# Optimization experiments

Measured on AMD Instinct MI355X. Metric: run time of the kernel, lower is better.

Reference implementation:

```python
import jax, jax.numpy as jnp
import numpy as np

N = 100000   # nodes
E = 1600000  # edges
G = 512      # graphs in batch
IN_C, H1, H2, OUT_C = 3, 64, 128, 2


def setup_inputs() -> dict:
    key = jax.random.key(0)
    ks = jax.random.split(key, 9)
    x = jax.random.normal(ks[0], (N, IN_C), dtype=jnp.float32)
    edge_index = jax.random.randint(ks[1], (2, E), 0, N, dtype=jnp.int64)
    batch = jnp.sort(jax.random.randint(ks[2], (N,), 0, G, dtype=jnp.int64))
    # Glorot-ish init for weights, zeros for biases (as PyG GCNConv / nn.Linear defaults roughly)
    def glorot(k, shape):
        lim = float(np.sqrt(6.0 / (shape[0] + shape[1])))
        return jax.random.uniform(k, shape, jnp.float32, -lim, lim)
    W1 = glorot(ks[3], (IN_C, H1)); b1 = jnp.zeros((H1,), jnp.float32)
    W2 = glorot(ks[4], (H1, H2));   b2 = jnp.zeros((H2,), jnp.float32)
    Wfc = glorot(ks[5], (H2, OUT_C)); bfc = jnp.zeros((OUT_C,), jnp.float32)
    return {"x": x, "edge_index": edge_index, "batch": batch,
            "W1": W1, "b1": b1, "W2": W2, "b2": b2, "Wfc": Wfc, "bfc": bfc}


def _gcn_conv(x, W, b, src, dst, dinv):
    # PyG GCNConv: out = D^{-1/2} (A + I) D^{-1/2} X W + b
    xw = x @ W                                    # [N, F]
    norm = dinv[src] * dinv[dst]                  # per-edge symmetric norm
    agg = jax.ops.segment_sum(norm[:, None] * xw[src], dst, num_segments=x.shape[0])
    agg = agg + (dinv * dinv)[:, None] * xw       # self-loop contribution
    return agg + b


def reference(x, edge_index, batch, W1, b1, W2, b2, Wfc, bfc):
    src, dst = edge_index[0], edge_index[1]
    # degree with self-loops (edge weight 1), counted at edge targets as in PyG
    deg = jax.ops.segment_sum(jnp.ones((E,), x.dtype), dst, num_segments=N) + 1.0
    dinv = jax.lax.rsqrt(deg)
    h = jax.nn.relu(_gcn_conv(x, W1, b1, src, dst, dinv))
    h = jax.nn.relu(_gcn_conv(h, W2, b2, src, dst, dinv))
    # global_mean_pool over batch indices
    sums = jax.ops.segment_sum(h, batch, num_segments=G)          # [G, H2]
    cnt = jax.ops.segment_sum(jnp.ones((N,), h.dtype), batch, num_segments=G)
    pooled = sums / jnp.maximum(cnt, 1.0)[:, None]
    return pooled @ Wfc + bfc
```

## Files before the change

### kernel.cpp

```cpp
#include <hip/hip_runtime.h>

#define NN 100000
#define NE 1600000
#define NG 512
#define C_H1 64
#define C_H2 128
#define C_OUT 2

#define MM2_BLOCKS ((NN + 127) / 128)
#define NB ((NN + 255) >> 8)
#define PCHUNKS 512
#define PCHUNK_E (NE / PCHUNKS)
#define AT_S 68

__global__ void k_hist(const int* __restrict__ ei, int* __restrict__ hist) {
    __shared__ int lh[NB];
    int tid = threadIdx.x;
    int blk = blockIdx.x;
    for (int i = tid; i < NB; i += 256) lh[i] = 0;
    __syncthreads();
    int base = blk * PCHUNK_E;
    for (int e = base + tid; e < base + PCHUNK_E; e += 256)
        atomicAdd(&lh[ei[NE + e] >> 8], 1);
    __syncthreads();
    for (int i = tid; i < NB; i += 256) hist[i * PCHUNKS + blk] = lh[i];
}

__global__ void k_colscan0(const int* __restrict__ hist, int* __restrict__ offs,
                           int* __restrict__ btot) {
    __shared__ int sh[256];
    int b = blockIdx.x;
    int tid = threadIdx.x;
    int v0 = hist[b * PCHUNKS + 2 * tid];
    int v1 = hist[b * PCHUNKS + 2 * tid + 1];
    sh[tid] = v0 + v1;
    __syncthreads();
    for (int off = 1; off < 256; off <<= 1) {
        int v = (tid >= off) ? sh[tid - off] : 0;
        __syncthreads();
        sh[tid] += v;
        __syncthreads();
    }
    int base = (tid == 0) ? 0 : sh[tid - 1];
    offs[b * PCHUNKS + 2 * tid]     = base;
    offs[b * PCHUNKS + 2 * tid + 1] = base + v0;
    if (tid == 255) btot[b] = sh[255];
}

__global__ void k_bbase(const int* __restrict__ btot, int* __restrict__ bbase,
                        int* __restrict__ row_ptr) {
    __shared__ int sh[256];
    int tid = threadIdx.x;
    int v0 = (2 * tid     < NB) ? btot[2 * tid]     : 0;
    int v1 = (2 * tid + 1 < NB) ? btot[2 * tid + 1] : 0;
    sh[tid] = v0 + v1;
    __syncthreads();
    for (int off = 1; off < 256; off <<= 1) {
        int v = (tid >= off) ? sh[tid - off] : 0;
        __syncthreads();
        sh[tid] += v;
        __syncthreads();
    }
    int base = (tid == 0) ? 0 : sh[tid - 1];
    if (2 * tid     < NB) bbase[2 * tid]     = base;
    if (2 * tid + 1 < NB) bbase[2 * tid + 1] = base + v0;
    if (tid == 255) { bbase[NB] = sh[255]; row_ptr[NN] = sh[255]; }
}

__global__ void k_scatterA(const int* __restrict__ ei, const int* __restrict__ offs,
                           const int* __restrict__ bbase, int2* __restrict__ ed2) {
    __shared__ int lcur[NB];
    int tid = threadIdx.x;
    int blk = blockIdx.x;
    for (int i = tid; i < NB; i += 256) lcur[i] = bbase[i] + offs[i * PCHUNKS + blk];
    __syncthreads();
    int base = blk * PCHUNK_E;
    for (int e = base + tid; e < base + PCHUNK_E; e += 256) {
        int s = ei[e], d = ei[NE + e];
        int pos = atomicAdd(&lcur[d >> 8], 1);
        int2 v; v.x = s; v.y = d;
        ed2[pos] = v;
    }
}

__global__ void k_B1(const int2* __restrict__ ed2, const int* __restrict__ bbase,
                     float* __restrict__ dinv, int* __restrict__ row_ptr) {
    __shared__ int ldeg[256];
    __shared__ int sh[256];
    int b = blockIdx.x;
    int tid = threadIdx.x;
    int lo = b << 8;
    ldeg[tid] = 0;
    __syncthreads();
    int beg = bbase[b], end = bbase[b + 1];
    for (int j = beg + tid; j < end; j += 256)
        atomicAdd(&ldeg[ed2[j].y - lo], 1);
    __syncthreads();
    int d = ldeg[tid];
    int node = lo + tid;
    if (node < NN) dinv[node] = rsqrtf((float)d + 1.0f);
    sh[tid] = d;
    __syncthreads();
    for (int off = 1; off < 256; off <<= 1) {
        int v = (tid >= off) ? sh[tid - off] : 0;
        __syncthreads();
        sh[tid] += v;
        __syncthreads();
    }
    int excl = beg + ((tid == 0) ? 0 : sh[tid - 1]);
    if (node < NN) row_ptr[node] = excl;
}

__global__ void k_x4(const float* __restrict__ x, float4* __restrict__ x4) {
    int n = blockIdx.x * blockDim.x + threadIdx.x;
    if (n >= NN) return;
    float4 v; v.x = x[n * 3]; v.y = x[n * 3 + 1]; v.z = x[n * 3 + 2]; v.w = 0.f;
    x4[n] = v;
}

__global__ void k_scatterB(const int* __restrict__ row_ptr, const int2* __restrict__ ed2,
                           const float* __restrict__ dinv, const float4* __restrict__ x4,
                           int2* __restrict__ ed, float4* __restrict__ aggx4) {
    __shared__ int   lcur[256];
    __shared__ float ldin[256];
    __shared__ float lax[256 * 3];
    int b = blockIdx.x;
    int lo = b << 8;
    int tid = threadIdx.x;
    int node = lo + tid;
    if (node <= NN) lcur[tid] = row_ptr[node < NN ? node : NN];
    else            lcur[tid] = 0;
    ldin[tid] = (node < NN) ? dinv[node] : 0.f;
    lax[tid] = 0.f; lax[256 + tid] = 0.f; lax[512 + tid] = 0.f;
    __syncthreads();
    int seg_beg = row_ptr[lo];
    int hi = lo + 256; if (hi > NN) hi = NN;
    int seg_end = row_ptr[hi];
    for (int j = seg_beg + tid; j < seg_end; j += 256) {
        int2 sd = ed2[j];
        int local = sd.y - lo;
        int pos = atomicAdd(&lcur[local], 1);
        float nrm = dinv[sd.x] * ldin[local];
        int2 v; v.x = sd.x; v.y = __float_as_int(nrm);
        ed[pos] = v;
        float4 xs = x4[sd.x];
        atomicAdd(&lax[local],       nrm * xs.x);
        atomicAdd(&lax[256 + local], nrm * xs.y);
        atomicAdd(&lax[512 + local], nrm * xs.z);
    }
    __syncthreads();
    if (node < NN) {
        float di = ldin[tid];
        float s2 = di * di;
        float4 xs = x4[node];
        float4 a;
        a.x = lax[tid]       + s2 * xs.x;
        a.y = lax[256 + tid] + s2 * xs.y;
        a.z = lax[512 + tid] + s2 * xs.z;
        a.w = 0.f;
        aggx4[node] = a;
    }
}

__global__ void k_edge1(const int* __restrict__ row_ptr, const int2* __restrict__ ed,
                        const float4* __restrict__ aggx4, const float* __restrict__ dinv,
                        const float* __restrict__ W1, const float* __restrict__ b1,
                        float* __restrict__ agg1) {
    __shared__ float4 lp[256];
    int t = blockIdx.x * 256 + threadIdx.x;
    int n = t >> 6, c = t & 63;
    int lane = threadIdx.x & 63;
    int wbase = threadIdx.x & 192;

    float w0 = W1[c], w1 = W1[64 + c], w2 = W1[128 + c], bb = b1[c];
    float4 an = aggx4[n];
    float di = dinv[n];
    float hself = fmaxf(fmaf(an.x, w0, fmaf(an.y, w1, fmaf(an.z, w2, bb))), 0.f);
    float acc = di * di * hself;

    int beg = row_ptr[n], end = row_ptr[n + 1];
    for (int base = beg; base < end; base += 64) {
        int m = end - base; if (m > 64) m = 64;
        if (lane < m) {
            int2 v = ed[base + lane];
            float4 ax = aggx4[v.x];
            float4 p; p.x = ax.x; p.y = ax.y; p.z = ax.z; p.w = __int_as_float(v.y);
            lp[wbase + lane] = p;
        }
        int e = 0;
        for (; e + 3 < m; e += 4) {
            float4 p0 = lp[wbase + e];
            float4 p1 = lp[wbase + e + 1];
            float4 p2 = lp[wbase + e + 2];
            float4 p3 = lp[wbase + e + 3];
            float h0  = fmaxf(fmaf(p0.x, w0, fmaf(p0.y, w1, fmaf(p0.z, w2, bb))), 0.f);
            float h1v = fmaxf(fmaf(p1.x, w0, fmaf(p1.y, w1, fmaf(p1.z, w2, bb))), 0.f);
            float h2v = fmaxf(fmaf(p2.x, w0, fmaf(p2.y, w1, fmaf(p2.z, w2, bb))), 0.f);
            float h3v = fmaxf(fmaf(p3.x, w0, fmaf(p3.y, w1, fmaf(p3.z, w2, bb))), 0.f);
            acc = fmaf(p0.w, h0, acc);
            acc = fmaf(p1.w, h1v, acc);
            acc = fmaf(p2.w, h2v, acc);
            acc = fmaf(p3.w, h3v, acc);
        }
        for (; e < m; ++e) {
            float4 p = lp[wbase + e];
            float h = fmaxf(fmaf(p.x, w0, fmaf(p.y, w1, fmaf(p.z, w2, bb))), 0.f);
            acc = fmaf(p.w, h, acc);
        }
    }
    agg1[t] = acc;
}

__global__ void k_mm2pool(const float* __restrict__ agg1, const float* __restrict__ W2,
                          const float* __restrict__ b2, const int* __restrict__ batch,
                          float* __restrict__ pooled) {
    __shared__ float wt[C_H1 * C_H2];
    __shared__ float at[128 * AT_S];
    __shared__ float lpool[4 * C_H2];
    int tid = threadIdx.x;
    {
        const float4* w4 = (const float4*)W2;
        float4* wl = (float4*)wt;
        for (int i = tid; i < (C_H1 * C_H2) / 4; i += 256) wl[i] = w4[i];
        const float4* a4 = (const float4*)(agg1 + (size_t)blockIdx.x * 128 * C_H1);
        for (int i = tid; i < 128 * 16; i += 256) {
            int row = i >> 4, k4 = i & 15;
            *(float4*)&at[row * AT_S + k4 * 4] = a4[i];
        }
        for (int i = tid; i < 4 * C_H2; i += 256) lpool[i] = 0.f;
    }
    __syncthreads();

    int tx = tid & 15;
    int my = tid >> 4;
    int c0 = tx * 8;
    int m0 = my * 8;

    float acc[8][8];
#pragma unroll
    for (int i = 0; i < 8; ++i)
#pragma unroll
        for (int j = 0; j < 8; ++j) acc[i][j] = 0.f;

    for (int k0 = 0; k0 < C_H1; k0 += 4) {
        float4 wf[4][2];
#pragma unroll
        for (int kk = 0; kk < 4; ++kk) {
            wf[kk][0] = *(const float4*)&wt[(k0 + kk) * C_H2 + c0];
            wf[kk][1] = *(const float4*)&wt[(k0 + kk) * C_H2 + c0 + 4];
        }
#pragma unroll
        for (int i = 0; i < 8; ++i) {
            float4 af = *(const float4*)&at[(m0 + i) * AT_S + k0];
#pragma unroll
            for (int kk = 0; kk < 4; ++kk) {
                float a = (kk == 0) ? af.x : (kk == 1) ? af.y : (kk == 2) ? af.z : af.w;
                acc[i][0] = fmaf(a, wf[kk][0].x, acc[i][0]);
                acc[i][1] = fmaf(a, wf[kk][0].y, acc[i][1]);
                acc[i][2] = fmaf(a, wf[kk][0].z, acc[i][2]);
                acc[i][3] = fmaf(a, wf[kk][0].w, acc[i][3]);
                acc[i][4] = fmaf(a, wf[kk][1].x, acc[i][4]);
                acc[i][5] = fmaf(a, wf[kk][1].y, acc[i][5]);
                acc[i][6] = fmaf(a, wf[kk][1].z, acc[i][6]);
                acc[i][7] = fmaf(a, wf[kk][1].w, acc[i][7]);
            }
        }
    }

    int nbase = blockIdx.x * 128 + m0;
    int gbase = batch[blockIdx.x * 128];
    int gidx[8];
#pragma unroll
    for (int i = 0; i < 8; ++i)
        gidx[i] = (nbase + i < NN) ? batch[nbase + i] : -1;
    float bias[8];
#pragma unroll
    for (int j = 0; j < 8; ++j) bias[j] = b2[c0 + j];

#pragma unroll
    for (int j = 0; j < 8; ++j) {
        int run_g = -1;
        float rs = 0.f;
#pragma unroll
        for (int i = 0; i < 8; ++i) {
            if (gidx[i] < 0) break;
            float h = fmaxf(acc[i][j] + bias[j], 0.f);
            if (gidx[i] != run_g) {
                if (run_g >= 0) {
                    int slot = run_g - gbase;
                    if (slot < 4) atomicAdd(&lpool[slot * C_H2 + c0 + j], rs);
                    else          atomicAdd(&pooled[(run_g << 7) + c0 + j], rs);
                }
                run_g = gidx[i]; rs = h;
            } else {
                rs += h;
            }
        }
        if (run_g >= 0) {
            int slot = run_g - gbase;
            if (slot < 4) atomicAdd(&lpool[slot * C_H2 + c0 + j], rs);
            else          atomicAdd(&pooled[(run_g << 7) + c0 + j], rs);
        }
    }
    __syncthreads();
    for (int i = tid; i < 4 * C_H2; i += 256) {
        int slot = i >> 7, c = i & 127;
        int g = gbase + slot;
        float v = lpool[i];
        if (g < NG && v != 0.f) atomicAdd(&pooled[(g << 7) + c], v);
    }
}

__device__ __forceinline__ int lower_bound(const int* __restrict__ a, int n, int key) {
    int lo = 0, hi = n;
    while (lo < hi) { int mid = (lo + hi) >> 1; if (a[mid] < key) lo = mid + 1; else hi = mid; }
    return lo;
}

__global__ void k_fc(const float* __restrict__ pooled, const int* __restrict__ batch,
                     const float* __restrict__ Wfc, const float* __restrict__ bfc,
                     float* __restrict__ out) {
    int t = blockIdx.x * blockDim.x + threadIdx.x;
    if (t >= NG * C_OUT) return;
    int g = t >> 1, o = t & 1;
    int start = lower_bound(batch, NN, g);
    int end   = lower_bound(batch, NN, g + 1);
    float inv = 1.f / fmaxf((float)(end - start), 1.f);
    float s = bfc[o];
    for (int cc = 0; cc < C_H2; ++cc)
        s = fmaf(pooled[(g << 7) + cc] * inv, Wfc[cc * C_OUT + o], s);
    out[t] = s;
}

extern "C" void kernel_launch(void* const* d_in, const int* in_sizes, int n_in,
                              void* d_out, int out_size, void* d_ws, size_t ws_size,
                              hipStream_t stream) {
    const float* x     = (const float*)d_in[0];
    const int*   ei    = (const int*)d_in[1];
    const int*   batch = (const int*)d_in[2];
    const float* W1    = (const float*)d_in[3];
    const float* b1    = (const float*)d_in[4];
    const float* W2    = (const float*)d_in[5];
    const float* b2    = (const float*)d_in[6];
    const float* Wfc   = (const float*)d_in[7];
    const float* bfc   = (const float*)d_in[8];
    float* out = (float*)d_out;

    char* p = (char*)d_ws;
    auto alloc = [&](size_t bytes) { char* r = p; p += (bytes + 255) & ~size_t(255); return r; };
    float*  dinv    = (float*) alloc((size_t)NN * 4);
    int*    row_ptr = (int*)   alloc((size_t)(NN + 1) * 4);
    int*    btot    = (int*)   alloc((size_t)NB * 4);
    int*    bbase   = (int*)   alloc((size_t)(NB + 1) * 4);
    int*    hist    = (int*)   alloc((size_t)NB * PCHUNKS * 4);
    int*    offs    = (int*)   alloc((size_t)NB * PCHUNKS * 4);
    int2*   ed2     = (int2*)  alloc((size_t)NE * 8);
    int2*   ed      = (int2*)  alloc((size_t)NE * 8);
    float4* x4      = (float4*)alloc((size_t)NN * 16);
    float4* aggx4   = (float4*)alloc((size_t)NN * 16);
    float*  agg1    = (float*) alloc((size_t)(NN + 128) * C_H1 * 4);
    float*  pooled  = (float*) alloc((size_t)NG * C_H2 * 4);

    hipMemsetAsync(pooled, 0, (size_t)NG * C_H2 * 4, stream);
    k_hist    <<<PCHUNKS, 256, 0, stream>>>(ei, hist);
    k_colscan0<<<NB, 256, 0, stream>>>(hist, offs, btot);
    k_bbase   <<<1, 256, 0, stream>>>(btot, bbase, row_ptr);
    k_scatterA<<<PCHUNKS, 256, 0, stream>>>(ei, offs, bbase, ed2);
    k_B1      <<<NB, 256, 0, stream>>>(ed2, bbase, dinv, row_ptr);
    k_x4      <<<(NN + 255) / 256, 256, 0, stream>>>(x, x4);
    k_scatterB<<<NB, 256, 0, stream>>>(row_ptr, ed2, dinv, x4, ed, aggx4);
    k_edge1   <<<(NN * C_H1) / 256, 256, 0, stream>>>(row_ptr, ed, aggx4, dinv, W1, b1, agg1);
    k_mm2pool <<<MM2_BLOCKS, 256, 0, stream>>>(agg1, W2, b2, batch, pooled);
    k_fc      <<<(NG * C_OUT + 255) / 256, 256, 0, stream>>>(pooled, batch, Wfc, bfc, out);
}
```

Before: 231.1 us.

## Widen bucket kernels to 1024 threads, pack dinv into x4, use readlane broadcast

k_B1 and k_scatterB now launch 1024 threads per block, so each 256-node bucket has four times as many threads streaming its edge list, with the per-node work guarded to the first 256 threads. dinv is packed into the w component of x4 and aggx4, which removes a separate dinv gather in scatterB and a dinv load in edge1. k_edge1 replaces its LDS staging buffer with wave-level readlane broadcasts of the gathered neighbor data. The readlane loop is serial over each 64-edge chunk and uses scalar instructions, and the larger blocks can reduce occupancy and add contention on the shared-memory atomics.

```diff
diff --git a/kernel.cpp b/kernel.cpp
--- a/kernel.cpp
+++ b/kernel.cpp
@@ -13,6 +13,10 @@
 #define PCHUNK_E (NE / PCHUNKS)
 #define AT_S 68
 
+__device__ __forceinline__ float bcast(float v, int lane) {
+    return __int_as_float(__builtin_amdgcn_readlane(__float_as_int(v), lane));
+}
+
 __global__ void k_hist(const int* __restrict__ ei, int* __restrict__ hist) {
     __shared__ int lh[NB];
     int tid = threadIdx.x;
@@ -90,31 +94,34 @@
     int b = blockIdx.x;
     int tid = threadIdx.x;
     int lo = b << 8;
-    ldeg[tid] = 0;
+    if (tid < 256) ldeg[tid] = 0;
     __syncthreads();
     int beg = bbase[b], end = bbase[b + 1];
-    for (int j = beg + tid; j < end; j += 256)
+    for (int j = beg + tid; j < end; j += 1024)
         atomicAdd(&ldeg[ed2[j].y - lo], 1);
     __syncthreads();
-    int d = ldeg[tid];
     int node = lo + tid;
-    if (node < NN) dinv[node] = rsqrtf((float)d + 1.0f);
-    sh[tid] = d;
+    if (tid < 256) {
+        int d = ldeg[tid];
+        if (node < NN) dinv[node] = rsqrtf((float)d + 1.0f);
+        sh[tid] = d;
+    }
     __syncthreads();
     for (int off = 1; off < 256; off <<= 1) {
-        int v = (tid >= off) ? sh[tid - off] : 0;
-        __syncthreads();
-        sh[tid] += v;
-        __syncthreads();
-    }
-    int excl = beg + ((tid == 0) ? 0 : sh[tid - 1]);
-    if (node < NN) row_ptr[node] = excl;
-}
-
-__global__ void k_x4(const float* __restrict__ x, float4* __restrict__ x4) {
+        int v = (tid < 256 && tid >= off) ? sh[tid - off] : 0;
+        __syncthreads();
+        if (tid < 256) sh[tid] += v;
+        __syncthreads();
+    }
+    if (tid < 256 && node < NN)
+        row_ptr[node] = beg + ((tid == 0) ? 0 : sh[tid - 1]);
+}
+
+__global__ void k_x4(const float* __restrict__ x, const float* __restrict__ dinv,
+                     float4* __restrict__ x4) {
     int n = blockIdx.x * blockDim.x + threadIdx.x;
     if (n >= NN) return;
-    float4 v; v.x = x[n * 3]; v.y = x[n * 3 + 1]; v.z = x[n * 3 + 2]; v.w = 0.f;
+    float4 v; v.x = x[n * 3]; v.y = x[n * 3 + 1]; v.z = x[n * 3 + 2]; v.w = dinv[n];
     x4[n] = v;
 }
 
@@ -128,28 +135,29 @@
     int lo = b << 8;
     int tid = threadIdx.x;
     int node = lo + tid;
-    if (node <= NN) lcur[tid] = row_ptr[node < NN ? node : NN];
-    else            lcur[tid] = 0;
-    ldin[tid] = (node < NN) ? dinv[node] : 0.f;
-    lax[tid] = 0.f; lax[256 + tid] = 0.f; lax[512 + tid] = 0.f;
+    if (tid < 256) {
+        lcur[tid] = row_ptr[node < NN ? node : NN];
+        ldin[tid] = (node < NN) ? dinv[node] : 0.f;
+    }
+    if (tid < 768) lax[tid] = 0.f;
     __syncthreads();
     int seg_beg = row_ptr[lo];
     int hi = lo + 256; if (hi > NN) hi = NN;
     int seg_end = row_ptr[hi];
-    for (int j = seg_beg + tid; j < seg_end; j += 256) {
+    for (int j = seg_beg + tid; j < seg_end; j += 1024) {
         int2 sd = ed2[j];
         int local = sd.y - lo;
         int pos = atomicAdd(&lcur[local], 1);
-        float nrm = dinv[sd.x] * ldin[local];
+        float4 xs = x4[sd.x];
+        float nrm = xs.w * ldin[local];
         int2 v; v.x = sd.x; v.y = __float_as_int(nrm);
         ed[pos] = v;
-        float4 xs = x4[sd.x];
         atomicAdd(&lax[local],       nrm * xs.x);
         atomicAdd(&lax[256 + local], nrm * xs.y);
         atomicAdd(&lax[512 + local], nrm * xs.z);
     }
     __syncthreads();
-    if (node < NN) {
+    if (tid < 256 && node < NN) {
         float di = ldin[tid];
         float s2 = di * di;
         float4 xs = x4[node];
@@ -157,55 +165,40 @@
         a.x = lax[tid]       + s2 * xs.x;
         a.y = lax[256 + tid] + s2 * xs.y;
         a.z = lax[512 + tid] + s2 * xs.z;
-        a.w = 0.f;
+        a.w = di;
         aggx4[node] = a;
     }
 }
 
 __global__ void k_edge1(const int* __restrict__ row_ptr, const int2* __restrict__ ed,
-                        const float4* __restrict__ aggx4, const float* __restrict__ dinv,
+                        const float4* __restrict__ aggx4,
                         const float* __restrict__ W1, const float* __restrict__ b1,
                         float* __restrict__ agg1) {
-    __shared__ float4 lp[256];
     int t = blockIdx.x * 256 + threadIdx.x;
     int n = t >> 6, c = t & 63;
     int lane = threadIdx.x & 63;
-    int wbase = threadIdx.x & 192;
 
     float w0 = W1[c], w1 = W1[64 + c], w2 = W1[128 + c], bb = b1[c];
     float4 an = aggx4[n];
-    float di = dinv[n];
     float hself = fmaxf(fmaf(an.x, w0, fmaf(an.y, w1, fmaf(an.z, w2, bb))), 0.f);
-    float acc = di * di * hself;
+    float acc = an.w * an.w * hself;
 
     int beg = row_ptr[n], end = row_ptr[n + 1];
     for (int base = beg; base < end; base += 64) {
         int m = end - base; if (m > 64) m = 64;
+        float px = 0.f, py = 0.f, pz = 0.f, pw = 0.f;
         if (lane < m) {
             int2 v = ed[base + lane];
             float4 ax = aggx4[v.x];
-            float4 p; p.x = ax.x; p.y = ax.y; p.z = ax.z; p.w = __int_as_float(v.y);
-            lp[wbase + lane] = p;
-        }
-        int e = 0;
-        for (; e + 3 < m; e += 4) {
-            float4 p0 = lp[wbase + e];
-            float4 p1 = lp[wbase + e + 1];
-            float4 p2 = lp[wbase + e + 2];
-            float4 p3 = lp[wbase + e + 3];
-            float h0  = fmaxf(fmaf(p0.x, w0, fmaf(p0.y, w1, fmaf(p0.z, w2, bb))), 0.f);
-            float h1v = fmaxf(fmaf(p1.x, w0, fmaf(p1.y, w1, fmaf(p1.z, w2, bb))), 0.f);
-            float h2v = fmaxf(fmaf(p2.x, w0, fmaf(p2.y, w1, fmaf(p2.z, w2, bb))), 0.f);
-            float h3v = fmaxf(fmaf(p3.x, w0, fmaf(p3.y, w1, fmaf(p3.z, w2, bb))), 0.f);
-            acc = fmaf(p0.w, h0, acc);
-            acc = fmaf(p1.w, h1v, acc);
-            acc = fmaf(p2.w, h2v, acc);
-            acc = fmaf(p3.w, h3v, acc);
-        }
-        for (; e < m; ++e) {
-            float4 p = lp[wbase + e];
-            float h = fmaxf(fmaf(p.x, w0, fmaf(p.y, w1, fmaf(p.z, w2, bb))), 0.f);
-            acc = fmaf(p.w, h, acc);
+            px = ax.x; py = ax.y; pz = ax.z; pw = __int_as_float(v.y);
+        }
+        for (int e = 0; e < m; ++e) {
+            float qx = bcast(px, e);
+            float qy = bcast(py, e);
+            float qz = bcast(pz, e);
+            float qw = bcast(pw, e);
+            float h = fmaxf(fmaf(qx, w0, fmaf(qy, w1, fmaf(qz, w2, bb))), 0.f);
+            acc = fmaf(qw, h, acc);
         }
     }
     agg1[t] = acc;
@@ -366,10 +359,10 @@
     k_colscan0<<<NB, 256, 0, stream>>>(hist, offs, btot);
     k_bbase   <<<1, 256, 0, stream>>>(btot, bbase, row_ptr);
     k_scatterA<<<PCHUNKS, 256, 0, stream>>>(ei, offs, bbase, ed2);
-    k_B1      <<<NB, 256, 0, stream>>>(ed2, bbase, dinv, row_ptr);
-    k_x4      <<<(NN + 255) / 256, 256, 0, stream>>>(x, x4);
-    k_scatterB<<<NB, 256, 0, stream>>>(row_ptr, ed2, dinv, x4, ed, aggx4);
-    k_edge1   <<<(NN * C_H1) / 256, 256, 0, stream>>>(row_ptr, ed, aggx4, dinv, W1, b1, agg1);
+    k_B1      <<<NB, 1024, 0, stream>>>(ed2, bbase, dinv, row_ptr);
+    k_x4      <<<(NN + 255) / 256, 256, 0, stream>>>(x, dinv, x4);
+    k_scatterB<<<NB, 1024, 0, stream>>>(row_ptr, ed2, dinv, x4, ed, aggx4);
+    k_edge1   <<<(NN * C_H1) / 256, 256, 0, stream>>>(row_ptr, ed, aggx4, W1, b1, agg1);
     k_mm2pool <<<MM2_BLOCKS, 256, 0, stream>>>(agg1, W2, b2, batch, pooled);
     k_fc      <<<(NG * C_OUT + 255) / 256, 256, 0, stream>>>(pooled, batch, Wfc, bfc, out);
 }
```

Result: slower. 246.7 us (+6.7%).
